# Kernel optimization log

Measured on AMD Instinct MI355X. Metric: run time of the kernel, lower is better.

Reference implementation:

```python
import jax, jax.numpy as jnp
import numpy as np

N, E, DIN, D, NUM_LAYERS = 50000, 800000, 64, 128, 3


def setup_inputs() -> dict:
    key = jax.random.key(0)
    ks = jax.random.split(key, 16)
    s = lambda fan_in: 1.0 / np.sqrt(fan_in)
    inp = {
        "x": jax.random.normal(ks[0], (N, DIN), jnp.float32),
        "edge_index": jax.random.randint(ks[1], (2, E), 0, N, jnp.int64),
        "edge_attr": jax.random.normal(ks[2], (E,), jnp.float32),
        "batch": jnp.zeros((N,), jnp.int64),
        # embed: Linear(DIN, D)
        "W_embed": jax.random.uniform(ks[3], (DIN, D), jnp.float32, -s(DIN), s(DIN)),
        "b_embed": jax.random.uniform(ks[4], (D,), jnp.float32, -s(DIN), s(DIN)),
        # msg_snd: Linear(D, D)
        "W_snd": jax.random.uniform(ks[5], (D, D), jnp.float32, -s(D), s(D)),
        "b_snd": jax.random.uniform(ks[6], (D,), jnp.float32, -s(D), s(D)),
        # msg_rec: Linear(2D, 2D)
        "W_rec": jax.random.uniform(ks[7], (2 * D, 2 * D), jnp.float32, -s(2 * D), s(2 * D)),
        "b_rec": jax.random.uniform(ks[8], (2 * D,), jnp.float32, -s(2 * D), s(2 * D)),
        # GRUCell(input=2D, hidden=D): gates ordered (r, z, n) as in torch
        "W_ih": jax.random.uniform(ks[9], (2 * D, 3 * D), jnp.float32, -s(D), s(D)),
        "b_ih": jax.random.uniform(ks[10], (3 * D,), jnp.float32, -s(D), s(D)),
        "W_hh": jax.random.uniform(ks[11], (D, 3 * D), jnp.float32, -s(D), s(D)),
        "b_hh": jax.random.uniform(ks[12], (3 * D,), jnp.float32, -s(D), s(D)),
    }
    return inp


def reference(x, edge_index, edge_attr, batch, W_embed, b_embed, W_snd, b_snd,
              W_rec, b_rec, W_ih, b_ih, W_hh, b_hh):
    n_nodes = x.shape[0]
    row, col = edge_index[0], edge_index[1]
    ea = edge_attr[:, None]                                    # [E,1]
    # scatter_mean denominator: in-degree, clamped to 1
    cnt = jax.ops.segment_sum(jnp.ones_like(edge_attr), col, num_segments=n_nodes)
    cnt = jnp.maximum(cnt, 1.0)[:, None]                       # [N,1]

    h = x @ W_embed + b_embed                                  # [N,D]
    for _ in range(NUM_LAYERS):
        s = jax.nn.leaky_relu(h @ W_snd + b_snd)               # msg_snd, [N,D]
        msgs = s[row] * ea                                     # gather + weight, [E,D]
        agg = jax.ops.segment_sum(msgs, col, num_segments=n_nodes) / cnt  # scatter_mean
        m = jax.nn.leaky_relu(jnp.concatenate([agg, h], -1) @ W_rec + b_rec)  # [N,2D]
        # torch GRUCell
        gi = m @ W_ih + b_ih                                   # [N,3D]
        gh = h @ W_hh + b_hh                                   # [N,3D]
        ir, iz, inn = jnp.split(gi, 3, axis=-1)
        hr, hz, hn = jnp.split(gh, 3, axis=-1)
        r = jax.nn.sigmoid(ir + hr)
        z = jax.nn.sigmoid(iz + hz)
        n = jnp.tanh(inn + r * hn)
        h = (1.0 - z) * n + z * h
    return h
```

## Files before the change

### kernel.cpp

```cpp
#include <hip/hip_runtime.h>
#include <hip/hip_bf16.h>
#include <stdint.h>

using bf16 = __hip_bfloat16;
typedef __attribute__((ext_vector_type(8))) short short8;
typedef __attribute__((ext_vector_type(4))) float f32x4;

#define LRELU_SLOPE 0.01f

#define GLOAD_LDS16(g, l) __builtin_amdgcn_global_load_lds( \
    (const __attribute__((address_space(1))) void*)(g),     \
    (__attribute__((address_space(3))) void*)(l), 16, 0, 0)

__device__ __forceinline__ float b2f(short s) {
    union { uint32_t u; float f; } cv;
    cv.u = ((uint32_t)(uint16_t)s) << 16;
    return cv.f;
}
__device__ __forceinline__ short f2b(float f) {
    bf16 h = __float2bfloat16(f);
    return *reinterpret_cast<short*>(&h);
}

__global__ __launch_bounds__(256) void gemm_m64_kernel(
    const bf16* __restrict__ A, int lda,
    const bf16* __restrict__ BT,
    const float* __restrict__ bias,
    bf16* __restrict__ C, int ldc,
    int N, int K, int cprShift, int act)
{
    __shared__ bf16 As[64 * 128];
    const int t   = threadIdx.x;
    const int wv  = t >> 6, ln = t & 63, m16 = ln & 15, q = ln >> 4;
    const int row0 = blockIdx.x * 64;
    const int col0 = (wv >> 1) * 64;
    const int wr   = (wv & 1) * 32;
    const int cmask = (1 << cprShift) - 1;
    const int trips = (1 << cprShift) >> 2;

    for (int i = 0; i < trips; ++i) {
        int g    = i * 256 + t;
        int row  = g >> cprShift;
        int cidx = (g & cmask) ^ (row & cmask);
        int grow = row0 + row; if (grow > N - 1) grow = N - 1;
        GLOAD_LDS16(A + (size_t)grow * lda + cidx * 8,
                    As + ((i * 256 + wv * 64) << 3));
    }
    __syncthreads();

    f32x4 acc[2][4];
#pragma unroll
    for (int mi = 0; mi < 2; ++mi)
#pragma unroll
        for (int ni = 0; ni < 4; ++ni)
            acc[mi][ni] = (f32x4){0.f, 0.f, 0.f, 0.f};

    for (int k0 = 0; k0 < K; k0 += 32) {
        int cbase = (k0 >> 3) + q;
        short8 a[2], b[4];
#pragma unroll
        for (int mi = 0; mi < 2; ++mi) {
            int row = wr + mi * 16 + m16;
            int cs  = cbase ^ (row & cmask);
            a[mi] = *reinterpret_cast<const short8*>(As + row * K + cs * 8);
        }
#pragma unroll
        for (int ni = 0; ni < 4; ++ni)
            b[ni] = *reinterpret_cast<const short8*>(
                BT + (size_t)(col0 + ni * 16 + m16) * K + k0 + q * 8);
#pragma unroll
        for (int mi = 0; mi < 2; ++mi)
#pragma unroll
            for (int ni = 0; ni < 4; ++ni)
                acc[mi][ni] = __builtin_amdgcn_mfma_f32_16x16x32_bf16(
                    a[mi], b[ni], acc[mi][ni], 0, 0, 0);
    }

#pragma unroll
    for (int mi = 0; mi < 2; ++mi) {
        int rbase = row0 + wr + mi * 16 + q * 4;
#pragma unroll
        for (int ni = 0; ni < 4; ++ni) {
            int col = col0 + ni * 16 + m16;
            float bv = bias[col];
#pragma unroll
            for (int r = 0; r < 4; ++r) {
                int row = rbase + r;
                if (row < N) {
                    float v = acc[mi][ni][r] + bv;
                    if (act) v = (v > 0.f) ? v : LRELU_SLOPE * v;
                    C[(size_t)row * ldc + col] = __float2bfloat16(v);
                }
            }
        }
    }
}

__global__ __launch_bounds__(256, 4) void layer_kernel(
    const bf16* __restrict__ cat,
    const bf16* __restrict__ WM,
    const float* __restrict__ bM,
    const bf16* __restrict__ WX,
    const float* __restrict__ bX,
    bf16* __restrict__ catH,
    float* __restrict__ out32,
    int N, int last)
{
    __shared__ bf16 smem[16384];
    bf16* CatA  = smem;
    bf16* CatHs = smem + 4096;
    bf16* Mlo   = smem + 8192;
    bf16* Mhi   = smem + 12288;

    const int t  = threadIdx.x;
    const int wv = t >> 6, ln = t & 63, m16 = ln & 15, q = ln >> 4;
    const int row0 = blockIdx.x * 32;

#pragma unroll
    for (int i = 0; i < 4; ++i) {
        int s    = i * 256 + t;
        int R    = s >> 9;
        int row  = (s >> 4) & 31;
        int c    = (s & 15) ^ (row & 15);
        int grow = row0 + row; if (grow > N - 1) grow = N - 1;
        GLOAD_LDS16(cat + (size_t)grow * 256 + R * 128 + c * 8,
                    smem + ((i * 256 + wv * 64) << 3));
    }
    __syncthreads();

    f32x4 macc[2][4];
#pragma unroll
    for (int mi = 0; mi < 2; ++mi)
#pragma unroll
        for (int ni = 0; ni < 4; ++ni)
            macc[mi][ni] = (f32x4){0.f, 0.f, 0.f, 0.f};

#pragma unroll
    for (int k0 = 0; k0 < 256; k0 += 32) {
        const bf16* Rg = (k0 < 128) ? CatA : CatHs;
        int kl = k0 & 127;
        short8 a[2], b[4];
#pragma unroll
        for (int mi = 0; mi < 2; ++mi) {
            int row = mi * 16 + m16;
            int c   = ((kl >> 3) + q) ^ m16;
            a[mi] = *reinterpret_cast<const short8*>(Rg + row * 128 + c * 8);
        }
#pragma unroll
        for (int ni = 0; ni < 4; ++ni)
            b[ni] = *reinterpret_cast<const short8*>(
                WM + (size_t)(wv * 64 + ni * 16 + m16) * 256 + k0 + q * 8);
#pragma unroll
        for (int mi = 0; mi < 2; ++mi)
#pragma unroll
            for (int ni = 0; ni < 4; ++ni)
                macc[mi][ni] = __builtin_amdgcn_mfma_f32_16x16x32_bf16(
                    a[mi], b[ni], macc[mi][ni], 0, 0, 0);
    }

#pragma unroll
    for (int mi = 0; mi < 2; ++mi) {
#pragma unroll
        for (int ni = 0; ni < 4; ++ni) {
            int ch  = wv * 64 + ni * 16 + m16;
            bf16* MR = (ch < 128) ? Mlo : Mhi;
            int chl = ch & 127;
            float bv = bM[ch];
#pragma unroll
            for (int r = 0; r < 4; ++r) {
                int row = mi * 16 + q * 4 + r;
                float v = macc[mi][ni][r] + bv;
                v = (v > 0.f) ? v : LRELU_SLOPE * v;
                int c = (chl >> 3) ^ (row & 15);
                short sv = f2b(v);
                MR[row * 128 + c * 8 + (chl & 7)] = *reinterpret_cast<bf16*>(&sv);
            }
        }
    }
    __syncthreads();

    f32x4 gr[2][2], gz[2][2], gn_[2][2], gh_[2][2];
#pragma unroll
    for (int mi = 0; mi < 2; ++mi)
#pragma unroll
        for (int ni = 0; ni < 2; ++ni) {
            gr[mi][ni]  = (f32x4){0.f, 0.f, 0.f, 0.f};
            gz[mi][ni]  = (f32x4){0.f, 0.f, 0.f, 0.f};
            gn_[mi][ni] = (f32x4){0.f, 0.f, 0.f, 0.f};
            gh_[mi][ni] = (f32x4){0.f, 0.f, 0.f, 0.f};
        }

#pragma unroll
    for (int k0 = 0; k0 < 256; k0 += 32) {
        const bf16* Rg = (k0 < 128) ? Mlo : Mhi;
        int kl = k0 & 127;
        short8 a[2];
#pragma unroll
        for (int mi = 0; mi < 2; ++mi) {
            int row = mi * 16 + m16;
            int c   = ((kl >> 3) + q) ^ m16;
            a[mi] = *reinterpret_cast<const short8*>(Rg + row * 128 + c * 8);
        }
        short8 br[2], bz[2], bn[2];
#pragma unroll
        for (int ni = 0; ni < 2; ++ni) {
            int cw = wv * 32 + ni * 16 + m16;
            br[ni] = *reinterpret_cast<const short8*>(WX + (size_t)(cw)       * 384 + k0 + q * 8);
            bz[ni] = *reinterpret_cast<const short8*>(WX + (size_t)(128 + cw) * 384 + k0 + q * 8);
            bn[ni] = *reinterpret_cast<const short8*>(WX + (size_t)(256 + cw) * 384 + k0 + q * 8);
        }
#pragma unroll
        for (int mi = 0; mi < 2; ++mi)
#pragma unroll
            for (int ni = 0; ni < 2; ++ni) {
                gr[mi][ni]  = __builtin_amdgcn_mfma_f32_16x16x32_bf16(a[mi], br[ni], gr[mi][ni], 0, 0, 0);
                gz[mi][ni]  = __builtin_amdgcn_mfma_f32_16x16x32_bf16(a[mi], bz[ni], gz[mi][ni], 0, 0, 0);
                gn_[mi][ni] = __builtin_amdgcn_mfma_f32_16x16x32_bf16(a[mi], bn[ni], gn_[mi][ni], 0, 0, 0);
            }
    }
#pragma unroll
    for (int k0 = 256; k0 < 384; k0 += 32) {
        int kl = k0 - 256;
        short8 a[2];
#pragma unroll
        for (int mi = 0; mi < 2; ++mi) {
            int row = mi * 16 + m16;
            int c   = ((kl >> 3) + q) ^ m16;
            a[mi] = *reinterpret_cast<const short8*>(CatHs + row * 128 + c * 8);
        }
        short8 br[2], bz[2], bh[2];
#pragma unroll
        for (int ni = 0; ni < 2; ++ni) {
            int cw = wv * 32 + ni * 16 + m16;
            br[ni] = *reinterpret_cast<const short8*>(WX + (size_t)(cw)       * 384 + k0 + q * 8);
            bz[ni] = *reinterpret_cast<const short8*>(WX + (size_t)(128 + cw) * 384 + k0 + q * 8);
            bh[ni] = *reinterpret_cast<const short8*>(WX + (size_t)(384 + cw) * 384 + k0 + q * 8);
        }
#pragma unroll
        for (int mi = 0; mi < 2; ++mi)
#pragma unroll
            for (int ni = 0; ni < 2; ++ni) {
                gr[mi][ni]  = __builtin_amdgcn_mfma_f32_16x16x32_bf16(a[mi], br[ni], gr[mi][ni], 0, 0, 0);
                gz[mi][ni]  = __builtin_amdgcn_mfma_f32_16x16x32_bf16(a[mi], bz[ni], gz[mi][ni], 0, 0, 0);
                gh_[mi][ni] = __builtin_amdgcn_mfma_f32_16x16x32_bf16(a[mi], bh[ni], gh_[mi][ni], 0, 0, 0);
            }
    }

#pragma unroll
    for (int mi = 0; mi < 2; ++mi) {
#pragma unroll
        for (int ni = 0; ni < 2; ++ni) {
            int ch = wv * 32 + ni * 16 + m16;
            float brv = bX[ch], bzv = bX[128 + ch];
            float bnv = bX[256 + ch], bhv = bX[384 + ch];
#pragma unroll
            for (int r = 0; r < 4; ++r) {
                int lrow = mi * 16 + q * 4 + r;
                int row  = row0 + lrow;
                if (row < N) {
                    int c = (ch >> 3) ^ (lrow & 15);
                    float hv = b2f(*reinterpret_cast<const short*>(
                        CatHs + lrow * 128 + c * 8 + (ch & 7)));
                    float rr = 1.f / (1.f + __expf(-(gr[mi][ni][r] + brv)));
                    float zz = 1.f / (1.f + __expf(-(gz[mi][ni][r] + bzv)));
                    float nn = tanhf(gn_[mi][ni][r] + bnv + rr * (gh_[mi][ni][r] + bhv));
                    float hnew = (1.f - zz) * nn + zz * hv;
                    short hb = f2b(hnew);
                    catH[(size_t)row * 256 + ch] = *reinterpret_cast<bf16*>(&hb);
                    if (last) out32[(size_t)row * 128 + ch] = hnew;
                }
            }
        }
    }
}

__global__ void prep_kernel(const float* __restrict__ x, bf16* __restrict__ xb, int nx,
                            const float* __restrict__ W_embed, bf16* __restrict__ TE,
                            const float* __restrict__ W_snd,   bf16* __restrict__ TS,
                            const float* __restrict__ W_rec,   bf16* __restrict__ TM,
                            const float* __restrict__ W_ih, const float* __restrict__ W_hh,
                            bf16* __restrict__ TX,
                            const float* __restrict__ b_ih, const float* __restrict__ b_hh,
                            float* __restrict__ bext)
{
    int t = blockIdx.x * 256 + threadIdx.x;
    if (t < nx) { xb[t] = __float2bfloat16(x[t]); return; }
    t -= nx;
    if (t < 8192)  { TE[(t % 128) * 64  + t / 128] = __float2bfloat16(W_embed[t]); return; }
    t -= 8192;
    if (t < 16384) { TS[(t % 128) * 128 + t / 128] = __float2bfloat16(W_snd[t]); return; }
    t -= 16384;
    if (t < 65536) { TM[(t % 256) * 256 + t / 256] = __float2bfloat16(W_rec[t]); return; }
    t -= 65536;
    if (t < 196608) {
        int c = t / 384, k = t - c * 384;
        float v;
        if (c < 256)      v = (k < 256) ? W_ih[k * 384 + c] : W_hh[(k - 256) * 384 + c];
        else if (c < 384) v = (k < 256) ? W_ih[k * 384 + c] : 0.f;
        else              v = (k < 256) ? 0.f : W_hh[(k - 256) * 384 + (c - 128)];
        TX[t] = __float2bfloat16(v);
        return;
    }
    t -= 196608;
    if (t < 512) {
        float v;
        if (t < 256)      v = b_ih[t] + b_hh[t];
        else if (t < 384) v = b_ih[t];
        else              v = b_hh[t - 128];
        bext[t] = v;
    }
}

__global__ void hist_kernel(const int* __restrict__ col, int* __restrict__ cnt, int E)
{
    int e = blockIdx.x * 256 + threadIdx.x;
    if (e < E) atomicAdd(&cnt[col[e]], 1);
}

__global__ void blockscan_kernel(const int* __restrict__ cnt, int* __restrict__ off,
                                 int* __restrict__ bsum, int N)
{
    __shared__ int sm[256];
    int i = blockIdx.x * 256 + threadIdx.x;
    int v = (i < N) ? cnt[i] : 0;
    sm[threadIdx.x] = v;
    __syncthreads();
    for (int d = 1; d < 256; d <<= 1) {
        int tv = (threadIdx.x >= (unsigned)d) ? sm[threadIdx.x - d] : 0;
        __syncthreads();
        sm[threadIdx.x] += tv;
        __syncthreads();
    }
    if (i < N) off[i] = sm[threadIdx.x] - v;
    if (threadIdx.x == 255) bsum[blockIdx.x] = sm[255];
}

__global__ void bscan_kernel(int* __restrict__ bsum, int nb)
{
    __shared__ int sm[512];
    int v = (threadIdx.x < (unsigned)nb) ? bsum[threadIdx.x] : 0;
    sm[threadIdx.x] = v;
    __syncthreads();
    for (int d = 1; d < 512; d <<= 1) {
        int tv = (threadIdx.x >= (unsigned)d) ? sm[threadIdx.x - d] : 0;
        __syncthreads();
        sm[threadIdx.x] += tv;
        __syncthreads();
    }
    if (threadIdx.x < (unsigned)nb) bsum[threadIdx.x] = sm[threadIdx.x] - v;
}

__global__ void addoff_kernel(int* __restrict__ off, const int* __restrict__ bsum,
                              const int* __restrict__ cnt, float* __restrict__ icnt,
                              int N, int E)
{
    int i = blockIdx.x * 256 + threadIdx.x;
    if (i < N) {
        off[i] += bsum[blockIdx.x];
        icnt[i] = 1.0f / fmaxf((float)cnt[i], 1.0f);
    }
    if (i == 0) off[N] = E;
}

__global__ void fill_kernel(const int* __restrict__ row, const int* __restrict__ col,
                            const float* __restrict__ ea, const int* __restrict__ off,
                            int* __restrict__ fil, int2* __restrict__ re, int E)
{
    int e = blockIdx.x * 256 + threadIdx.x;
    if (e < E) {
        int c = col[e];
        int p = atomicAdd(&fil[c], 1);
        int2 v; v.x = row[e]; v.y = __float_as_int(ea[e]);
        re[off[c] + p] = v;
    }
}

__global__ void agg_kernel(const int* __restrict__ off,
                           const int2* __restrict__ re,
                           const bf16* __restrict__ s,
                           const float* __restrict__ icnt,
                           bf16* __restrict__ cat, int N)
{
    int wid  = (int)((blockIdx.x * blockDim.x + threadIdx.x) >> 6);
    int lane = threadIdx.x & 63;
    if (wid >= N) return;
    const int rg = lane >> 4;
    const int cl = lane & 15;
    int b = off[wid], e = off[wid + 1];

    float acc[8];
#pragma unroll
    for (int j = 0; j < 8; ++j) acc[j] = 0.f;

    int i = b + rg;
    for (; i + 4 < e; i += 8) {
        int2 p0 = re[i];
        int2 p1 = re[i + 4];
        short8 v0 = *reinterpret_cast<const short8*>(s + (size_t)p0.x * 128 + cl * 8);
        short8 v1 = *reinterpret_cast<const short8*>(s + (size_t)p1.x * 128 + cl * 8);
        float w0 = __int_as_float(p0.y), w1 = __int_as_float(p1.y);
#pragma unroll
        for (int j = 0; j < 8; ++j) acc[j] += w0 * b2f(v0[j]) + w1 * b2f(v1[j]);
    }
    if (i < e) {
        int2 p0 = re[i];
        float w0 = __int_as_float(p0.y);
        short8 v0 = *reinterpret_cast<const short8*>(s + (size_t)p0.x * 128 + cl * 8);
#pragma unroll
        for (int j = 0; j < 8; ++j) acc[j] += w0 * b2f(v0[j]);
    }
#pragma unroll
    for (int j = 0; j < 8; ++j) {
        acc[j] += __shfl_xor(acc[j], 16, 64);
        acc[j] += __shfl_xor(acc[j], 32, 64);
    }
    if (rg == 0) {
        float ic = icnt[wid];
        short8 o;
#pragma unroll
        for (int j = 0; j < 8; ++j) o[j] = f2b(acc[j] * ic);
        *reinterpret_cast<short8*>(cat + (size_t)wid * 256 + cl * 8) = o;
    }
}

extern "C" void kernel_launch(void* const* d_in, const int* in_sizes, int n_in,
                              void* d_out, int out_size, void* d_ws, size_t ws_size,
                              hipStream_t stream)
{
    const float* x       = (const float*)d_in[0];
    const int*   ei      = (const int*)d_in[1];
    const float* ea      = (const float*)d_in[2];
    const float* W_embed = (const float*)d_in[4];
    const float* b_embed = (const float*)d_in[5];
    const float* W_snd   = (const float*)d_in[6];
    const float* b_snd   = (const float*)d_in[7];
    const float* W_rec   = (const float*)d_in[8];
    const float* b_rec   = (const float*)d_in[9];
    const float* W_ih    = (const float*)d_in[10];
    const float* b_ih    = (const float*)d_in[11];
    const float* W_hh    = (const float*)d_in[12];
    const float* b_hh    = (const float*)d_in[13];

    const int N = in_sizes[3];
    const int E = in_sizes[2];
    const int N64 = ((N + 63) / 64) * 64;

    char* p = (char*)d_ws;
    auto carve = [&](size_t bytes) {
        char* r = p;
        p += (bytes + 255) & ~(size_t)255;
        return (void*)r;
    };
    bf16*  xb   = (bf16*) carve((size_t)N64 * 64  * 2);
    bf16*  cat  = (bf16*) carve((size_t)N64 * 256 * 2);
    bf16*  sbuf = (bf16*) carve((size_t)N64 * 128 * 2);
    int2*  re   = (int2*) carve((size_t)E * 8);
    int*   cnt  = (int*)  carve((size_t)N * 4);
    int*   fil  = (int*)  carve((size_t)N * 4);
    int*   off  = (int*)  carve((size_t)(N + 1) * 4);
    int*   bsum = (int*)  carve((size_t)512 * 4);
    float* icnt = (float*)carve((size_t)N * 4);
    bf16*  wtE  = (bf16*) carve((size_t)128 * 64 * 2);
    bf16*  wtS  = (bf16*) carve((size_t)128 * 128 * 2);
    bf16*  wtM  = (bf16*) carve((size_t)256 * 256 * 2);
    bf16*  wtX  = (bf16*) carve((size_t)512 * 384 * 2);
    float* bext = (float*)carve((size_t)512 * 4);

    const int* rowp = ei;
    const int* colp = ei + E;

    hipMemsetAsync(cnt, 0, (size_t)N * 4, stream);
    hipMemsetAsync(fil, 0, (size_t)N * 4, stream);

    const int TB = 256;
    auto nb = [](int n) { return (n + 255) / 256; };

    prep_kernel<<<nb(N * 64 + 287232), TB, 0, stream>>>(
        x, xb, N * 64, W_embed, wtE, W_snd, wtS, W_rec, wtM,
        W_ih, W_hh, wtX, b_ih, b_hh, bext);

    hist_kernel<<<nb(E), TB, 0, stream>>>(colp, cnt, E);
    blockscan_kernel<<<nb(N), TB, 0, stream>>>(cnt, off, bsum, N);
    bscan_kernel<<<1, 512, 0, stream>>>(bsum, nb(N));
    addoff_kernel<<<nb(N), TB, 0, stream>>>(off, bsum, cnt, icnt, N, E);
    fill_kernel<<<nb(E), TB, 0, stream>>>(rowp, colp, ea, off, fil, re, E);

    const int gx  = (N + 63) / 64;
    const int gx2 = (N + 31) / 32;

    gemm_m64_kernel<<<gx, TB, 0, stream>>>(xb, 64, wtE, b_embed,
                                           cat + 128, 256, N, 64, 3, 0);

    for (int L = 0; L < 3; ++L) {
        gemm_m64_kernel<<<gx, TB, 0, stream>>>(cat + 128, 256, wtS, b_snd,
                                               sbuf, 128, N, 128, 4, 1);
        agg_kernel<<<(N * 64 + TB - 1) / TB, TB, 0, stream>>>(off, re, sbuf,
                                                              icnt, cat, N);
        layer_kernel<<<gx2, TB, 0, stream>>>(cat, wtM, b_rec, wtX, bext,
                                             cat + 128, (float*)d_out,
                                             N, (L == 2) ? 1 : 0);
    }
}
```

Before: 649.5 us.

## Double layer kernel row tile and stage outputs through LDS for coalesced stores

The fused layer kernel now handles 64 rows per block instead of 32, so each block reads its global weight fragments once for twice as many rows. Both the GEMM and layer kernels now write results into swizzled LDS first and then store them in coalesced 16-byte vectors instead of scattered 2-byte stores. The cost is more LDS per block (48KB), more accumulator registers, a dropped occupancy hint and extra barriers, which may lower occupancy. The final fp32 output is now built from bf16-rounded values, which slightly reduces its precision.

```diff
diff --git a/kernel.cpp b/kernel.cpp
--- a/kernel.cpp
+++ b/kernel.cpp
@@ -75,28 +75,40 @@
                 acc[mi][ni] = __builtin_amdgcn_mfma_f32_16x16x32_bf16(
                     a[mi], b[ni], acc[mi][ni], 0, 0, 0);
     }
+    __syncthreads();
 
 #pragma unroll
     for (int mi = 0; mi < 2; ++mi) {
-        int rbase = row0 + wr + mi * 16 + q * 4;
 #pragma unroll
         for (int ni = 0; ni < 4; ++ni) {
             int col = col0 + ni * 16 + m16;
             float bv = bias[col];
 #pragma unroll
             for (int r = 0; r < 4; ++r) {
-                int row = rbase + r;
-                if (row < N) {
-                    float v = acc[mi][ni][r] + bv;
-                    if (act) v = (v > 0.f) ? v : LRELU_SLOPE * v;
-                    C[(size_t)row * ldc + col] = __float2bfloat16(v);
-                }
+                int lrow = wr + mi * 16 + q * 4 + r;
+                float v = acc[mi][ni][r] + bv;
+                if (act) v = (v > 0.f) ? v : LRELU_SLOPE * v;
+                short sv = f2b(v);
+                As[lrow * 128 + (((col >> 3) ^ (lrow & 15)) << 3) + (col & 7)] =
+                    *reinterpret_cast<bf16*>(&sv);
             }
         }
     }
-}
-
-__global__ __launch_bounds__(256, 4) void layer_kernel(
+    __syncthreads();
+#pragma unroll
+    for (int i = 0; i < 4; ++i) {
+        int s   = i * 256 + t;
+        int row = s >> 4, c = s & 15;
+        int grow = row0 + row;
+        if (grow < N) {
+            short8 v = *reinterpret_cast<const short8*>(
+                As + row * 128 + ((c ^ (row & 15)) << 3));
+            *reinterpret_cast<short8*>(C + (size_t)grow * ldc + c * 8) = v;
+        }
+    }
+}
+
+__global__ __launch_bounds__(256) void layer_kernel(
     const bf16* __restrict__ cat,
     const bf16* __restrict__ WM,
     const float* __restrict__ bM,
@@ -106,21 +118,20 @@
     float* __restrict__ out32,
     int N, int last)
 {
-    __shared__ bf16 smem[16384];
-    bf16* CatA  = smem;
-    bf16* CatHs = smem + 4096;
-    bf16* Mlo   = smem + 8192;
-    bf16* Mhi   = smem + 12288;
+    __shared__ bf16 smem[24576];
+    bf16* R0 = smem;
+    bf16* R1 = smem + 8192;
+    bf16* R2 = smem + 16384;
 
     const int t  = threadIdx.x;
     const int wv = t >> 6, ln = t & 63, m16 = ln & 15, q = ln >> 4;
-    const int row0 = blockIdx.x * 32;
-
-#pragma unroll
-    for (int i = 0; i < 4; ++i) {
+    const int row0 = blockIdx.x * 64;
+
+#pragma unroll
+    for (int i = 0; i < 8; ++i) {
         int s    = i * 256 + t;
-        int R    = s >> 9;
-        int row  = (s >> 4) & 31;
+        int R    = s >> 10;
+        int row  = (s >> 4) & 63;
         int c    = (s & 15) ^ (row & 15);
         int grow = row0 + row; if (grow > N - 1) grow = N - 1;
         GLOAD_LDS16(cat + (size_t)grow * 256 + R * 128 + c * 8,
@@ -128,20 +139,20 @@
     }
     __syncthreads();
 
-    f32x4 macc[2][4];
-#pragma unroll
-    for (int mi = 0; mi < 2; ++mi)
+    f32x4 macc[4][4];
+#pragma unroll
+    for (int mi = 0; mi < 4; ++mi)
 #pragma unroll
         for (int ni = 0; ni < 4; ++ni)
             macc[mi][ni] = (f32x4){0.f, 0.f, 0.f, 0.f};
 
 #pragma unroll
     for (int k0 = 0; k0 < 256; k0 += 32) {
-        const bf16* Rg = (k0 < 128) ? CatA : CatHs;
+        const bf16* Rg = (k0 < 128) ? R0 : R1;
         int kl = k0 & 127;
-        short8 a[2], b[4];
-#pragma unroll
-        for (int mi = 0; mi < 2; ++mi) {
+        short8 a[4], b[4];
+#pragma unroll
+        for (int mi = 0; mi < 4; ++mi) {
             int row = mi * 16 + m16;
             int c   = ((kl >> 3) + q) ^ m16;
             a[mi] = *reinterpret_cast<const short8*>(Rg + row * 128 + c * 8);
@@ -151,19 +162,20 @@
             b[ni] = *reinterpret_cast<const short8*>(
                 WM + (size_t)(wv * 64 + ni * 16 + m16) * 256 + k0 + q * 8);
 #pragma unroll
-        for (int mi = 0; mi < 2; ++mi)
+        for (int mi = 0; mi < 4; ++mi)
 #pragma unroll
             for (int ni = 0; ni < 4; ++ni)
                 macc[mi][ni] = __builtin_amdgcn_mfma_f32_16x16x32_bf16(
                     a[mi], b[ni], macc[mi][ni], 0, 0, 0);
     }
-
-#pragma unroll
-    for (int mi = 0; mi < 2; ++mi) {
+    __syncthreads();
+
+#pragma unroll
+    for (int mi = 0; mi < 4; ++mi) {
 #pragma unroll
         for (int ni = 0; ni < 4; ++ni) {
             int ch  = wv * 64 + ni * 16 + m16;
-            bf16* MR = (ch < 128) ? Mlo : Mhi;
+            bf16* MR = (ch < 128) ? R0 : R2;
             int chl = ch & 127;
             float bv = bM[ch];
 #pragma unroll
@@ -171,17 +183,17 @@
                 int row = mi * 16 + q * 4 + r;
                 float v = macc[mi][ni][r] + bv;
                 v = (v > 0.f) ? v : LRELU_SLOPE * v;
-                int c = (chl >> 3) ^ (row & 15);
                 short sv = f2b(v);
-                MR[row * 128 + c * 8 + (chl & 7)] = *reinterpret_cast<bf16*>(&sv);
+                MR[row * 128 + (((chl >> 3) ^ (row & 15)) << 3) + (chl & 7)] =
+                    *reinterpret_cast<bf16*>(&sv);
             }
         }
     }
     __syncthreads();
 
-    f32x4 gr[2][2], gz[2][2], gn_[2][2], gh_[2][2];
-#pragma unroll
-    for (int mi = 0; mi < 2; ++mi)
+    f32x4 gr[4][2], gz[4][2], gn_[4][2], gh_[4][2];
+#pragma unroll
+    for (int mi = 0; mi < 4; ++mi)
 #pragma unroll
         for (int ni = 0; ni < 2; ++ni) {
             gr[mi][ni]  = (f32x4){0.f, 0.f, 0.f, 0.f};
@@ -192,11 +204,11 @@
 
 #pragma unroll
     for (int k0 = 0; k0 < 256; k0 += 32) {
-        const bf16* Rg = (k0 < 128) ? Mlo : Mhi;
+        const bf16* Rg = (k0 < 128) ? R0 : R2;
         int kl = k0 & 127;
-        short8 a[2];
-#pragma unroll
-        for (int mi = 0; mi < 2; ++mi) {
+        short8 a[4];
+#pragma unroll
+        for (int mi = 0; mi < 4; ++mi) {
             int row = mi * 16 + m16;
             int c   = ((kl >> 3) + q) ^ m16;
             a[mi] = *reinterpret_cast<const short8*>(Rg + row * 128 + c * 8);
@@ -210,7 +222,7 @@
             bn[ni] = *reinterpret_cast<const short8*>(WX + (size_t)(256 + cw) * 384 + k0 + q * 8);
         }
 #pragma unroll
-        for (int mi = 0; mi < 2; ++mi)
+        for (int mi = 0; mi < 4; ++mi)
 #pragma unroll
             for (int ni = 0; ni < 2; ++ni) {
                 gr[mi][ni]  = __builtin_amdgcn_mfma_f32_16x16x32_bf16(a[mi], br[ni], gr[mi][ni], 0, 0, 0);
@@ -221,12 +233,12 @@
 #pragma unroll
     for (int k0 = 256; k0 < 384; k0 += 32) {
         int kl = k0 - 256;
-        short8 a[2];
-#pragma unroll
-        for (int mi = 0; mi < 2; ++mi) {
+        short8 a[4];
+#pragma unroll
+        for (int mi = 0; mi < 4; ++mi) {
             int row = mi * 16 + m16;
             int c   = ((kl >> 3) + q) ^ m16;
-            a[mi] = *reinterpret_cast<const short8*>(CatHs + row * 128 + c * 8);
+            a[mi] = *reinterpret_cast<const short8*>(R1 + row * 128 + c * 8);
         }
         short8 br[2], bz[2], bh[2];
 #pragma unroll
@@ -237,7 +249,7 @@
             bh[ni] = *reinterpret_cast<const short8*>(WX + (size_t)(384 + cw) * 384 + k0 + q * 8);
         }
 #pragma unroll
-        for (int mi = 0; mi < 2; ++mi)
+        for (int mi = 0; mi < 4; ++mi)
 #pragma unroll
             for (int ni = 0; ni < 2; ++ni) {
                 gr[mi][ni]  = __builtin_amdgcn_mfma_f32_16x16x32_bf16(a[mi], br[ni], gr[mi][ni], 0, 0, 0);
@@ -245,9 +257,10 @@
                 gh_[mi][ni] = __builtin_amdgcn_mfma_f32_16x16x32_bf16(a[mi], bh[ni], gh_[mi][ni], 0, 0, 0);
             }
     }
-
-#pragma unroll
-    for (int mi = 0; mi < 2; ++mi) {
+    __syncthreads();
+
+#pragma unroll
+    for (int mi = 0; mi < 4; ++mi) {
 #pragma unroll
         for (int ni = 0; ni < 2; ++ni) {
             int ch = wv * 32 + ni * 16 + m16;
@@ -256,19 +269,37 @@
 #pragma unroll
             for (int r = 0; r < 4; ++r) {
                 int lrow = mi * 16 + q * 4 + r;
-                int row  = row0 + lrow;
-                if (row < N) {
-                    int c = (ch >> 3) ^ (lrow & 15);
-                    float hv = b2f(*reinterpret_cast<const short*>(
-                        CatHs + lrow * 128 + c * 8 + (ch & 7)));
-                    float rr = 1.f / (1.f + __expf(-(gr[mi][ni][r] + brv)));
-                    float zz = 1.f / (1.f + __expf(-(gz[mi][ni][r] + bzv)));
-                    float nn = tanhf(gn_[mi][ni][r] + bnv + rr * (gh_[mi][ni][r] + bhv));
-                    float hnew = (1.f - zz) * nn + zz * hv;
-                    short hb = f2b(hnew);
-                    catH[(size_t)row * 256 + ch] = *reinterpret_cast<bf16*>(&hb);
-                    if (last) out32[(size_t)row * 128 + ch] = hnew;
-                }
+                int c = ((ch >> 3) ^ (lrow & 15)) << 3;
+                float hv = b2f(*reinterpret_cast<const short*>(
+                    R1 + lrow * 128 + c + (ch & 7)));
+                float rr = 1.f / (1.f + __expf(-(gr[mi][ni][r] + brv)));
+                float zz = 1.f / (1.f + __expf(-(gz[mi][ni][r] + bzv)));
+                float nn = tanhf(gn_[mi][ni][r] + bnv + rr * (gh_[mi][ni][r] + bhv));
+                float hnew = (1.f - zz) * nn + zz * hv;
+                short hb = f2b(hnew);
+                R0[lrow * 128 + c + (ch & 7)] = *reinterpret_cast<bf16*>(&hb);
+            }
+        }
+    }
+    __syncthreads();
+
+#pragma unroll
+    for (int i = 0; i < 4; ++i) {
+        int s   = i * 256 + t;
+        int row = s >> 4, c = s & 15;
+        int grow = row0 + row;
+        if (grow < N) {
+            short8 v = *reinterpret_cast<const short8*>(
+                R0 + row * 128 + ((c ^ (row & 15)) << 3));
+            if (last) {
+                f32x4 lo, hi;
+#pragma unroll
+                for (int j = 0; j < 4; ++j) { lo[j] = b2f(v[j]); hi[j] = b2f(v[j + 4]); }
+                float* dst = out32 + (size_t)grow * 128 + c * 8;
+                *reinterpret_cast<f32x4*>(dst)     = lo;
+                *reinterpret_cast<f32x4*>(dst + 4) = hi;
+            } else {
+                *reinterpret_cast<short8*>(catH + (size_t)grow * 256 + c * 8) = v;
             }
         }
     }
@@ -485,8 +516,7 @@
     addoff_kernel<<<nb(N), TB, 0, stream>>>(off, bsum, cnt, icnt, N, E);
     fill_kernel<<<nb(E), TB, 0, stream>>>(rowp, colp, ea, off, fil, re, E);
 
-    const int gx  = (N + 63) / 64;
-    const int gx2 = (N + 31) / 32;
+    const int gx = (N + 63) / 64;
 
     gemm_m64_kernel<<<gx, TB, 0, stream>>>(xb, 64, wtE, b_embed,
                                            cat + 128, 256, N, 64, 3, 0);
@@ -496,8 +526,8 @@
                                                sbuf, 128, N, 128, 4, 1);
         agg_kernel<<<(N * 64 + TB - 1) / TB, TB, 0, stream>>>(off, re, sbuf,
                                                               icnt, cat, N);
-        layer_kernel<<<gx2, TB, 0, stream>>>(cat, wtM, b_rec, wtX, bext,
-                                             cat + 128, (float*)d_out,
-                                             N, (L == 2) ? 1 : 0);
-    }
-}
+        layer_kernel<<<gx, TB, 0, stream>>>(cat, wtM, b_rec, wtX, bext,
+                                            cat + 128, (float*)d_out,
+                                            N, (L == 2) ? 1 : 0);
+    }
+}
```

New measurement: 587.6 us. 1.11x faster.
